# Performance work log

Measured on AMD Instinct MI355X. Metric: run time of the kernel, lower is better.

## Reference

```python
import jax, jax.numpy as jnp
import numpy as np

# Model dims (see init_kwargs)
B, S, D = 2, 2048, 2048          # batch, seq, hidden
H, HD = 16, 128                  # heads, head_dim (= ND + RD)
ND, RD = 64, 64                  # nope dim, rope dim per head
R = 512                          # kv lora rank
THETA = 10000.0


def _rotate_half(x):
    # interleaved rotation: pairs (x0,x1) -> (-x1, x0)
    x1 = x[..., ::2]
    x2 = x[..., 1::2]
    return jnp.stack((-x2, x1), axis=-1).reshape(x.shape)


def apply_rope(x, positions):
    # x: [..., seq, dim]
    dim = x.shape[-1]
    freqs = 1.0 / THETA ** (jnp.arange(0, dim, 2, dtype=x.dtype) / dim)  # [dim/2]
    angles = positions.astype(x.dtype)[:, None] * freqs                  # [seq, dim/2]
    cos = jnp.repeat(jnp.cos(angles), 2, axis=-1)[None, None]            # [1,1,seq,dim]
    sin = jnp.repeat(jnp.sin(angles), 2, axis=-1)[None, None]
    return x * cos + _rotate_half(x) * sin


def setup_inputs() -> dict:
    key = jax.random.key(0)
    ks = jax.random.split(key, 7)
    def lin(k, out_f, in_f):  # torch Linear convention: weight [out, in]
        return jax.random.normal(k, (out_f, in_f), dtype=jnp.float32) * (in_f ** -0.5)
    return {
        "x": jax.random.normal(ks[0], (B, S, D), dtype=jnp.float32),
        "wq": lin(ks[1], D, D),
        "w_kv_down": lin(ks[2], R, D),
        "w_k_up": lin(ks[3], H * ND, R),
        "w_k_rope": lin(ks[4], RD, D),
        "w_v_up": lin(ks[5], D, R),
        "wo": lin(ks[6], D, D),
    }


def reference(x, wq, w_kv_down, w_k_up, w_k_rope, w_v_up, wo):
    b, s, _ = x.shape
    pos = jnp.arange(s)
    scale = 1.0 / np.sqrt(HD).astype(np.float32)

    # queries: [b,H,s,HD] split into nope/rope parts, rope applied per head
    q = (x @ wq.T).reshape(b, s, H, HD).transpose(0, 2, 1, 3)
    q_nope = q[..., :ND]
    q_rope = apply_rope(q[..., ND:], pos)

    # compressed kv latent: [b,s,R]
    c_kv = x @ w_kv_down.T
    k_nope = (c_kv @ w_k_up.T).reshape(b, s, H, ND).transpose(0, 2, 1, 3)  # [b,H,s,ND]
    k_rope = apply_rope((x @ w_k_rope.T)[:, None], pos)[:, 0]             # [b,s,RD], shared across heads
    v = (c_kv @ w_v_up.T).reshape(b, s, H, HD).transpose(0, 2, 1, 3)      # [b,H,s,HD]

    # decomposed scores: nope part (per head) + rope part (shared k)
    scores = jnp.einsum('bhqd,bhkd->bhqk', q_nope, k_nope)
    scores = scores + jnp.einsum('bhqd,bkd->bhqk', q_rope, k_rope)
    scores = scores * scale

    causal = jnp.tril(jnp.ones((s, s), dtype=bool))
    scores = jnp.where(causal[None, None], scores, jnp.finfo(scores.dtype).min)
    attn = jax.nn.softmax(scores, axis=-1)

    out = jnp.einsum('bhqk,bhkd->bhqd', attn, v)
    out = out.transpose(0, 2, 1, 3).reshape(b, s, D)
    return out @ wo.T
```

## Files before the change

kernel.cpp:

```cpp
#include <hip/hip_runtime.h>
#include <stdint.h>


typedef unsigned short u16;
typedef __bf16 bf16x8 __attribute__((ext_vector_type(8)));
typedef float f32x4 __attribute__((ext_vector_type(4)));

#define QLD 2816

__device__ __forceinline__ float bf2f(u16 u) {
    union { unsigned int i; float f; } x; x.i = ((unsigned int)u) << 16; return x.f;
}
__device__ __forceinline__ u16 f2bf(float f) {
    union { float f; unsigned int i; } x; x.f = f;
    unsigned int r = x.i + 0x7fffu + ((x.i >> 16) & 1u);
    return (u16)(r >> 16);
}
__device__ __forceinline__ void store_c(u16* p, float v)  { *p = f2bf(v); }
__device__ __forceinline__ void store_c(float* p, float v){ *p = v; }

#define GLOBAL_AS __attribute__((address_space(1)))
#define LDS_AS    __attribute__((address_space(3)))
__device__ __forceinline__ void gl_lds16(const void* g, void* l) {
    __builtin_amdgcn_global_load_lds((GLOBAL_AS const void*)g, (LDS_AS void*)l, 16, 0, 0);
}

#if __has_builtin(__builtin_amdgcn_exp2f)
__device__ __forceinline__ float exp2fast(float x) { return __builtin_amdgcn_exp2f(x); }
#else
__device__ __forceinline__ float exp2fast(float x) { return __expf(x * 0.6931471805599453f); }
#endif

template<int CTRL>
__device__ __forceinline__ float fmax_dpp(float v) {
    int s = __builtin_bit_cast(int, v);
    int t = __builtin_amdgcn_update_dpp(s, s, CTRL, 0xF, 0xF, true);
    return fmaxf(v, __builtin_bit_cast(float, t));
}
__device__ __forceinline__ float rowmax16(float v) {
    v = fmax_dpp<0xB1>(v);
    v = fmax_dpp<0x4E>(v);
    v = fmax_dpp<0x124>(v);
    v = fmax_dpp<0x128>(v);
    return v;
}

__device__ __forceinline__ void cv8(const float* __restrict__ src,
                                    u16* __restrict__ dst, int i) {
    const float4* s = (const float4*)src;
    float4 v0 = s[2*i], v1 = s[2*i + 1];
    union { u16 u[8]; uint4 v; } o;
    o.u[0] = f2bf(v0.x); o.u[1] = f2bf(v0.y); o.u[2] = f2bf(v0.z); o.u[3] = f2bf(v0.w);
    o.u[4] = f2bf(v1.x); o.u[5] = f2bf(v1.y); o.u[6] = f2bf(v1.z); o.u[7] = f2bf(v1.w);
    *((uint4*)(dst + 8*i)) = o.v;
}

__global__ void convert_all(const float* __restrict__ s_x,
                            const float* __restrict__ s_wq,
                            const float* __restrict__ s_kvd,
                            const float* __restrict__ s_kup,
                            const float* __restrict__ s_vup,
                            const float* __restrict__ s_kr,
                            u16* __restrict__ xc, u16* __restrict__ wqcat,
                            u16* __restrict__ kupc, u16* __restrict__ vupc) {
    int i = blockIdx.x * 256 + threadIdx.x;
    if      (i < 1048576) cv8(s_x,   xc,                          i);
    else if (i < 1572864) cv8(s_wq,  wqcat,                       i - 1048576);
    else if (i < 1703936) cv8(s_kvd, wqcat + (size_t)2112*2048,   i - 1572864);
    else if (i < 1769472) cv8(s_kup, kupc,                        i - 1703936);
    else if (i < 1900544) cv8(s_vup, vupc,                        i - 1769472);
    else if (i < 1916928) cv8(s_kr,  wqcat + (size_t)2048*2048,   i - 1900544);
}

template<typename CT>
__global__ __launch_bounds__(512, 2)
void gemm256(const u16* __restrict__ A, const u16* __restrict__ W,
             CT* __restrict__ C, int K, int lda, int ldw, int ldc) {
    __shared__ u16 lds[4][16384];
    const int tid  = threadIdx.x;
    const int lane = tid & 63, l15 = lane & 15, quad = lane >> 4;
    const int wave = tid >> 6;
    const int wr = wave >> 2, wc = wave & 3;
    const int bm = blockIdx.y * 256;
    const int bn = blockIdx.x * 256;

    const int R = tid >> 2, slot = tid & 3;
    const int k16 = slot ^ ((R >> 1) & 3);
    const u16* asrc = A + (size_t)(bm + R) * lda + k16 * 8;
    const u16* bsrc = W + (size_t)(bn + R) * ldw + k16 * 8;
    const size_t astep = (size_t)128 * lda;
    const size_t bstep = (size_t)128 * ldw;

    #define STAGE256(st, bi) { \
        const u16* a0_ = asrc + (size_t)(st) * 32; \
        const u16* b0_ = bsrc + (size_t)(st) * 32; \
        gl_lds16(a0_,         &lds[bi][tid * 8]); \
        gl_lds16(a0_ + astep, &lds[bi][(tid + 512) * 8]); \
        gl_lds16(b0_,         &lds[bi][(tid + 1024) * 8]); \
        gl_lds16(b0_ + bstep, &lds[bi][(tid + 1536) * 8]); \
    }

    const f32x4 fzero = {0.f, 0.f, 0.f, 0.f};
    f32x4 acc[8][4];
    #pragma unroll
    for (int i = 0; i < 8; ++i)
        #pragma unroll
        for (int j = 0; j < 4; ++j) acc[i][j] = fzero;

    const int aswz = (quad ^ ((l15 >> 1) & 3)) * 8;

    const int nst = K >> 5;
    STAGE256(0, 0)
    STAGE256(1, 1)
    STAGE256(2, 2)
    asm volatile("s_waitcnt vmcnt(8)" ::: "memory");
    __builtin_amdgcn_s_barrier();

    for (int t = 0; t < nst; ++t) {
        const u16* buf = lds[t & 3];
        bf16x8 af[8], bfv[4];
        #pragma unroll
        for (int mf = 0; mf < 8; ++mf)
            af[mf] = *reinterpret_cast<const bf16x8*>(
                &buf[(wr*128 + mf*16 + l15)*32 + aswz]);
        #pragma unroll
        for (int nf = 0; nf < 4; ++nf)
            bfv[nf] = *reinterpret_cast<const bf16x8*>(
                &buf[8192 + (wc*64 + nf*16 + l15)*32 + aswz]);
        int st = t + 3; if (st > nst - 1) st = nst - 1;
        STAGE256(st, (t + 3) & 3)
        __builtin_amdgcn_s_setprio(1);
        #pragma unroll
        for (int mf = 0; mf < 8; ++mf)
            #pragma unroll
            for (int nf = 0; nf < 4; ++nf)
                acc[mf][nf] = __builtin_amdgcn_mfma_f32_16x16x32_bf16(
                    af[mf], bfv[nf], acc[mf][nf], 0, 0, 0);
        __builtin_amdgcn_s_setprio(0);
        asm volatile("s_waitcnt vmcnt(8) lgkmcnt(0)" ::: "memory");
        __builtin_amdgcn_sched_barrier(0);
        __builtin_amdgcn_s_barrier();
        __builtin_amdgcn_sched_barrier(0);
    }
    #undef STAGE256

    #pragma unroll
    for (int mf = 0; mf < 8; ++mf)
        #pragma unroll
        for (int nf = 0; nf < 4; ++nf)
            #pragma unroll
            for (int r = 0; r < 4; ++r) {
                int gm = bm + wr*128 + mf*16 + quad*4 + r;
                int gn = bn + wc*64 + nf*16 + l15;
                store_c(&C[(size_t)gm * ldc + gn], acc[mf][nf][r]);
            }
}

template<int EPI, typename CT>
__device__ __forceinline__ void gemm128_body(
        u16 (*lds)[12288],
        const u16* __restrict__ A, const u16* __restrict__ W,
        CT* __restrict__ C, int K, int lda, int ldw, int ldc,
        int bm, int bn) {
    const int tid  = threadIdx.x;
    const int lane = tid & 63, l15 = lane & 15, quad = lane >> 4;
    const int wave = tid >> 6;
    const int wr = wave >> 2, wc = wave & 3;

    const int R = tid >> 2, slot = tid & 3;
    const int k16 = slot ^ ((R >> 1) & 3);
    const u16* asrc = A + (size_t)(bm + R) * lda + k16 * 8;
    const u16* bsrc = W + (size_t)(bn + R) * ldw + k16 * 8;
    const size_t bstep = (size_t)128 * ldw;

    #define STAGE128(st, bi) { \
        const u16* a0_ = asrc + (size_t)(st) * 32; \
        const u16* b0_ = bsrc + (size_t)(st) * 32; \
        gl_lds16(a0_,         &lds[bi][tid * 8]); \
        gl_lds16(b0_,         &lds[bi][(tid + 512) * 8]); \
        gl_lds16(b0_ + bstep, &lds[bi][(tid + 1024) * 8]); \
    }

    const f32x4 fzero = {0.f, 0.f, 0.f, 0.f};
    f32x4 acc[4][4];
    #pragma unroll
    for (int i = 0; i < 4; ++i)
        #pragma unroll
        for (int j = 0; j < 4; ++j) acc[i][j] = fzero;

    const int aswz = (quad ^ ((l15 >> 1) & 3)) * 8;

    const int nst = K >> 5;
    STAGE128(0, 0)
    STAGE128(1, 1)
    asm volatile("s_waitcnt vmcnt(3)" ::: "memory");
    __builtin_amdgcn_s_barrier();

    int b0 = 0, bs = 2;
    for (int t = 0; t < nst; ++t) {
        const u16* buf = lds[b0];
        bf16x8 af[4], bfv[4];
        #pragma unroll
        for (int mf = 0; mf < 4; ++mf)
            af[mf] = *reinterpret_cast<const bf16x8*>(
                &buf[(wr*64 + mf*16 + l15)*32 + aswz]);
        #pragma unroll
        for (int nf = 0; nf < 4; ++nf)
            bfv[nf] = *reinterpret_cast<const bf16x8*>(
                &buf[4096 + (wc*64 + nf*16 + l15)*32 + aswz]);
        int st = t + 2; if (st > nst - 1) st = nst - 1;
        STAGE128(st, bs)
        __builtin_amdgcn_s_setprio(1);
        #pragma unroll
        for (int mf = 0; mf < 4; ++mf)
            #pragma unroll
            for (int nf = 0; nf < 4; ++nf)
                acc[mf][nf] = __builtin_amdgcn_mfma_f32_16x16x32_bf16(
                    af[mf], bfv[nf], acc[mf][nf], 0, 0, 0);
        __builtin_amdgcn_s_setprio(0);
        asm volatile("s_waitcnt vmcnt(3) lgkmcnt(0)" ::: "memory");
        __builtin_amdgcn_sched_barrier(0);
        __builtin_amdgcn_s_barrier();
        __builtin_amdgcn_sched_barrier(0);
        b0 = (b0 == 2) ? 0 : b0 + 1;
        bs = (bs == 2) ? 0 : bs + 1;
    }
    #undef STAGE128

    #pragma unroll
    for (int mf = 0; mf < 4; ++mf)
        #pragma unroll
        for (int nf = 0; nf < 4; ++nf)
            #pragma unroll
            for (int r = 0; r < 4; ++r) {
                int gm = bm + wr*64 + mf*16 + quad*4 + r;
                int gn = bn + wc*64 + nf*16 + l15;
                size_t ci;
                if (EPI == 1) ci = (size_t)gm*ldc + ((gn >> 6)*128 + (gn & 63));
                else          ci = (size_t)gm*ldc + gn;
                store_c(&C[ci], acc[mf][nf][r]);
            }
}

template<typename CT>
__global__ __launch_bounds__(512, 4)
void gemm128(const u16* __restrict__ A, const u16* __restrict__ W,
             CT* __restrict__ C, int K, int lda, int ldw, int ldc) {
    __shared__ u16 lds[3][12288];
    gemm128_body<0>(lds, A, W, C, K, lda, ldw, ldc,
                    (int)blockIdx.y * 128, (int)blockIdx.x * 256);
}

__global__ __launch_bounds__(512, 4)
void kv_up(const u16* __restrict__ ckv, const u16* __restrict__ kupc,
           u16* __restrict__ keff, const u16* __restrict__ vupc,
           u16* __restrict__ vT) {
    __shared__ u16 lds[3][12288];
    const int bx = blockIdx.x;
    if (bx < 128) {
        int bn = (bx & 3) * 256, bm = (bx >> 2) * 128;
        gemm128_body<1>(lds, ckv, kupc, keff, 512, QLD, 512, 2048, bm, bn);
    } else {
        int b2 = bx - 128;
        int bn = (b2 & 15) * 256, bm = (b2 >> 4) * 128;
        gemm128_body<0>(lds, vupc, ckv, vT, 512, 512, QLD, 4096, bm, bn);
    }
}

__global__ void rope_woc(u16* __restrict__ qcat, u16* __restrict__ keff,
                         const float* __restrict__ wo_src, u16* __restrict__ woc) {
    const int blk = blockIdx.x;
    if (blk >= 512) {
        int i = (blk - 512) * 256 + threadIdx.x;
        cv8(wo_src, woc, i);
        return;
    }
    int idx = blk * 256 + threadIdx.x;
    int i = idx & 31, r = idx >> 5;
    int pos = r & 2047;
    float freq = powf(10000.0f, -(float)i * (1.0f/32.0f));
    float ang  = (float)pos * freq;
    float s = sinf(ang), c = cosf(ang);

    u16* row = qcat + (size_t)r * QLD + 64 + 2*i;
    #pragma unroll
    for (int h = 0; h < 16; ++h) {
        unsigned int* p = (unsigned int*)(row + h*128);
        unsigned int v = *p;
        float x0 = bf2f((u16)(v & 0xffffu)), x1 = bf2f((u16)(v >> 16));
        unsigned int lo = f2bf(x0*c - x1*s);
        unsigned int hi = f2bf(x1*c + x0*s);
        *p = lo | (hi << 16);
    }

    const u16* p = qcat + (size_t)r * QLD + 2048 + 2*i;
    float x0 = bf2f(p[0]), x1 = bf2f(p[1]);
    union { u16 u[2]; unsigned int w; } o;
    o.u[0] = f2bf(x0*c - x1*s);
    o.u[1] = f2bf(x1*c + x0*s);
    unsigned int* base = (unsigned int*)(keff + (size_t)r*2048 + 64 + 2*i);
    #pragma unroll
    for (int h = 0; h < 16; ++h) base[h*64] = o.w;
}

__global__ __launch_bounds__(256, 3)
void attn_kernel(u16* __restrict__ qcat, const u16* __restrict__ KE,
                 const u16* __restrict__ VT) {
    constexpr int S = 2048;
    const int L = (int)blockIdx.y * 16 + (int)blockIdx.x;
    const int xcd = L & 7, j = L >> 3;
    const int bh   = xcd * 4 + (j & 3);
    const int pair = j >> 2;
    const int b = bh >> 4, h = bh & 15;

    __shared__ u16 Ks[64*128];
    __shared__ u16 Vs[128*64];
    __shared__ u16 Ps[64*68];

    const int tid  = threadIdx.x;
    const int lane = tid & 63, l15 = lane & 15, quad = lane >> 4;
    const int wave = tid >> 6;

    const u16* ksrc[4];
    const u16* vsrc[4];
    #pragma unroll
    for (int i = 0; i < 4; ++i) {
        int g = tid + i*256;
        {
            int r = g >> 4, slot = g & 15, cg = slot ^ (r & 15);
            ksrc[i] = KE + (size_t)(b*S + r)*2048 + h*128 + cg*8;
        }
        {
            int d = g >> 3, slot = g & 7, cg = slot ^ (d & 7);
            vsrc[i] = VT + (size_t)(h*128 + d)*4096 + (size_t)(b*S) + cg*8;
        }
    }

    bf16x8 kreg[4], vreg[4];
    #pragma unroll
    for (int i = 0; i < 4; ++i) {
        kreg[i] = *reinterpret_cast<const bf16x8*>(ksrc[i]);
        vreg[i] = *reinterpret_cast<const bf16x8*>(vsrc[i]);
    }

    union { u16 u[8]; bf16x8 v; } onesu;
    #pragma unroll
    for (int i = 0; i < 8; ++i) onesu.u[i] = 0x3f80;
    const bf16x8 ones = onesu.v;

    const f32x4 fzero = {0.f, 0.f, 0.f, 0.f};
    const float NEG = -1e30f;
    const float KLOG = 0.12751739f;
    const float THR = 8.0f;

    __bf16* PsB = reinterpret_cast<__bf16*>(Ps);

    for (int half = 0; half < 2; ++half) {
        const int qt = half ? pair : 31 - pair;
        const int nkt = qt + 1;

        u16* qbase = qcat + (size_t)(b*S + qt*64) * QLD + h*128;
        bf16x8 aq[4];
        #pragma unroll
        for (int ks = 0; ks < 4; ++ks)
            aq[ks] = *reinterpret_cast<const bf16x8*>(
                qbase + (size_t)(wave*16 + l15)*QLD + ks*32 + quad*8);

        float m2[4]  = {NEG, NEG, NEG, NEG};
        float l_i[4] = {0.f, 0.f, 0.f, 0.f};
        f32x4 oacc[8];
        #pragma unroll
        for (int i = 0; i < 8; ++i) oacc[i] = fzero;

        const int qrow0 = qt*64 + wave*16 + quad*4;

        for (int kt = 0; kt < nkt; ++kt) {
            const bool is_last = (kt == nkt - 1);
            #pragma unroll
            for (int i = 0; i < 4; ++i) {
                *reinterpret_cast<bf16x8*>(&Ks[(tid + i*256) * 8]) = kreg[i];
                *reinterpret_cast<bf16x8*>(&Vs[(tid + i*256) * 8]) = vreg[i];
            }
            {
                int ktn = (kt + 1 < nkt) ? kt + 1 : 0;
                #pragma unroll
                for (int i = 0; i < 4; ++i) {
                    kreg[i] = *reinterpret_cast<const bf16x8*>(ksrc[i] + (size_t)ktn*(64*2048));
                    vreg[i] = *reinterpret_cast<const bf16x8*>(vsrc[i] + (size_t)ktn*64);
                }
            }
            __syncthreads();

            f32x4 sfr[4];
            __builtin_amdgcn_s_setprio(1);
            #pragma unroll
            for (int nt = 0; nt < 4; ++nt) {
                f32x4 s = fzero;
                int n = nt*16 + l15;
                #pragma unroll
                for (int ks = 0; ks < 4; ++ks) {
                    int c = ks*4 + quad;
                    bf16x8 bk = *reinterpret_cast<const bf16x8*>(&Ks[n*128 + ((c ^ l15) * 8)]);
                    s = __builtin_amdgcn_mfma_f32_16x16x32_bf16(aq[ks], bk, s, 0, 0, 0);
                }
                sfr[nt] = s;
            }
            __builtin_amdgcn_s_setprio(0);
            if (is_last) {
                #pragma unroll
                for (int nt = 0; nt < 4; ++nt) {
                    int kg = kt*64 + nt*16 + l15;
                    #pragma unroll
                    for (int r = 0; r < 4; ++r)
                        if (kg > qrow0 + r) sfr[nt][r] = NEG;
                }
            }
            float rm[4];
            #pragma unroll
            for (int r = 0; r < 4; ++r) {
                rm[r] = fmaxf(fmaxf(sfr[0][r], sfr[1][r]), fmaxf(sfr[2][r], sfr[3][r]));
                rm[r] = rowmax16(rm[r]);
            }
            float c2[4];
            int need = 0;
            #pragma unroll
            for (int r = 0; r < 4; ++r) {
                c2[r] = rm[r] * KLOG;
                need |= (c2[r] > m2[r] + THR) ? 1 : 0;
            }
            if (__any(need)) {
                float alpha[4];
                #pragma unroll
                for (int r = 0; r < 4; ++r) {
                    float mn = fmaxf(m2[r], c2[r]);
                    alpha[r] = exp2fast(m2[r] - mn);
                    m2[r] = mn;
                    l_i[r] *= alpha[r];
                }
                #pragma unroll
                for (int i = 0; i < 8; ++i)
                    #pragma unroll
                    for (int r = 0; r < 4; ++r)
                        oacc[i][r] *= alpha[r];
            }
            float pf[4][4];
            #pragma unroll
            for (int nt = 0; nt < 4; ++nt)
                #pragma unroll
                for (int r = 0; r < 4; ++r)
                    pf[nt][r] = exp2fast(__builtin_fmaf(sfr[nt][r], KLOG, -m2[r]));

            #pragma unroll
            for (int nt = 0; nt < 4; ++nt) {
                int base = (wave*16 + quad*4)*68 + nt*16 + l15;
                #pragma unroll
                for (int r = 0; r < 4; ++r)
                    PsB[base + r*68] = (__bf16)pf[nt][r];
            }

            f32x4 lfr = fzero;
            __builtin_amdgcn_s_setprio(1);
            #pragma unroll
            for (int ks = 0; ks < 2; ++ks) {
                bf16x8 pa = *reinterpret_cast<const bf16x8*>(
                    &Ps[(wave*16 + l15)*68 + ks*32 + quad*8]);
                lfr = __builtin_amdgcn_mfma_f32_16x16x32_bf16(pa, ones, lfr, 0, 0, 0);
                #pragma unroll
                for (int ntv = 0; ntv < 8; ++ntv) {
                    int c = ks*4 + quad;
                    bf16x8 bv = *reinterpret_cast<const bf16x8*>(
                        &Vs[(ntv*16 + l15)*64 + ((c ^ (l15 & 7)) * 8)]);
                    oacc[ntv] = __builtin_amdgcn_mfma_f32_16x16x32_bf16(pa, bv, oacc[ntv], 0, 0, 0);
                }
            }
            __builtin_amdgcn_s_setprio(0);
            #pragma unroll
            for (int r = 0; r < 4; ++r) l_i[r] += lfr[r];
            __syncthreads();
        }

        #pragma unroll
        for (int r = 0; r < 4; ++r) {
            float inv = 1.0f / l_i[r];
            int qrow = wave*16 + quad*4 + r;
            #pragma unroll
            for (int ntv = 0; ntv < 8; ++ntv) {
                int d = ntv*16 + l15;
                qbase[(size_t)qrow*QLD + d] = f2bf(oacc[ntv][r] * inv);
            }
        }
    }
}

extern "C" void kernel_launch(void* const* d_in, const int* in_sizes, int n_in,
                              void* d_out, int out_size, void* d_ws, size_t ws_size,
                              hipStream_t stream) {
    (void)in_sizes; (void)n_in; (void)out_size; (void)ws_size;
    float* out = (float*)d_out;
    char* ws = (char*)d_ws;

    u16* xc     = (u16*)(ws);
    u16* qcat   = (u16*)(ws + 16777216);
    u16* keff   = (u16*)(ws + 39845888);
    u16* wqcat  = (u16*)(ws + 56623104);
    u16* kupc   = (u16*)(ws + 68157440);
    u16* vupc   = (u16*)(ws + 69206016);
    u16* vT     = xc;
    u16* woc    = wqcat;

    convert_all<<<7488, 256, 0, stream>>>(
        (const float*)d_in[0], (const float*)d_in[1], (const float*)d_in[2],
        (const float*)d_in[3], (const float*)d_in[5], (const float*)d_in[4],
        xc, wqcat, kupc, vupc);

    gemm256<u16><<<dim3(11, 16), 512, 0, stream>>>(
        xc, wqcat, qcat, 2048, 2048, 2048, QLD);

    rope_woc<<<2560, 256, 0, stream>>>(qcat, keff, (const float*)d_in[6], woc);

    kv_up<<<384, 512, 0, stream>>>(qcat + 2112, kupc, keff, vupc, vT);

    attn_kernel<<<dim3(16, 32), 256, 0, stream>>>(qcat, keff, vT);

    gemm128<float><<<dim3(8, 32), 512, 0, stream>>>(
        qcat, woc, out, 2048, QLD, 2048, 2048);
}
```

Before: 310.5 us.

## Load V fragments directly from global into registers, dropping LDS staging of V

```diff
diff --git a/kernel.cpp b/kernel.cpp
--- a/kernel.cpp
+++ b/kernel.cpp
@@ -303,7 +303,7 @@
     for (int h = 0; h < 16; ++h) base[h*64] = o.w;
 }
 
-__global__ __launch_bounds__(256, 3)
+__global__ __launch_bounds__(256, 2)
 void attn_kernel(u16* __restrict__ qcat, const u16* __restrict__ KE,
                  const u16* __restrict__ VT) {
     constexpr int S = 2048;
@@ -314,7 +314,6 @@
     const int b = bh >> 4, h = bh & 15;
 
     __shared__ u16 Ks[64*128];
-    __shared__ u16 Vs[128*64];
     __shared__ u16 Ps[64*68];
 
     const int tid  = threadIdx.x;
@@ -322,26 +321,19 @@
     const int wave = tid >> 6;
 
     const u16* ksrc[4];
-    const u16* vsrc[4];
     #pragma unroll
     for (int i = 0; i < 4; ++i) {
         int g = tid + i*256;
-        {
-            int r = g >> 4, slot = g & 15, cg = slot ^ (r & 15);
-            ksrc[i] = KE + (size_t)(b*S + r)*2048 + h*128 + cg*8;
-        }
-        {
-            int d = g >> 3, slot = g & 7, cg = slot ^ (d & 7);
-            vsrc[i] = VT + (size_t)(h*128 + d)*4096 + (size_t)(b*S) + cg*8;
-        }
-    }
-
-    bf16x8 kreg[4], vreg[4];
-    #pragma unroll
-    for (int i = 0; i < 4; ++i) {
+        int r = g >> 4, slot = g & 15, cg = slot ^ (r & 15);
+        ksrc[i] = KE + (size_t)(b*S + r)*2048 + h*128 + cg*8;
+    }
+
+    const u16* vb = VT + (size_t)(h*128 + l15)*4096 + (size_t)(b*S) + quad*8;
+
+    bf16x8 kreg[4];
+    #pragma unroll
+    for (int i = 0; i < 4; ++i)
         kreg[i] = *reinterpret_cast<const bf16x8*>(ksrc[i]);
-        vreg[i] = *reinterpret_cast<const bf16x8*>(vsrc[i]);
-    }
 
     union { u16 u[8]; bf16x8 v; } onesu;
     #pragma unroll
@@ -377,17 +369,22 @@
         for (int kt = 0; kt < nkt; ++kt) {
             const bool is_last = (kt == nkt - 1);
             #pragma unroll
-            for (int i = 0; i < 4; ++i) {
+            for (int i = 0; i < 4; ++i)
                 *reinterpret_cast<bf16x8*>(&Ks[(tid + i*256) * 8]) = kreg[i];
-                *reinterpret_cast<bf16x8*>(&Vs[(tid + i*256) * 8]) = vreg[i];
-            }
+
+            bf16x8 vfr[2][8];
+            #pragma unroll
+            for (int ks = 0; ks < 2; ++ks)
+                #pragma unroll
+                for (int ntv = 0; ntv < 8; ++ntv)
+                    vfr[ks][ntv] = *reinterpret_cast<const bf16x8*>(
+                        vb + (size_t)ntv*65536 + kt*64 + ks*32);
+
             {
                 int ktn = (kt + 1 < nkt) ? kt + 1 : 0;
                 #pragma unroll
-                for (int i = 0; i < 4; ++i) {
+                for (int i = 0; i < 4; ++i)
                     kreg[i] = *reinterpret_cast<const bf16x8*>(ksrc[i] + (size_t)ktn*(64*2048));
-                    vreg[i] = *reinterpret_cast<const bf16x8*>(vsrc[i] + (size_t)ktn*64);
-                }
             }
             __syncthreads();
 
@@ -466,12 +463,9 @@
                     &Ps[(wave*16 + l15)*68 + ks*32 + quad*8]);
                 lfr = __builtin_amdgcn_mfma_f32_16x16x32_bf16(pa, ones, lfr, 0, 0, 0);
                 #pragma unroll
-                for (int ntv = 0; ntv < 8; ++ntv) {
-                    int c = ks*4 + quad;
-                    bf16x8 bv = *reinterpret_cast<const bf16x8*>(
-                        &Vs[(ntv*16 + l15)*64 + ((c ^ (l15 & 7)) * 8)]);
-                    oacc[ntv] = __builtin_amdgcn_mfma_f32_16x16x32_bf16(pa, bv, oacc[ntv], 0, 0, 0);
-                }
+                for (int ntv = 0; ntv < 8; ++ntv)
+                    oacc[ntv] = __builtin_amdgcn_mfma_f32_16x16x32_bf16(
+                        pa, vfr[ks][ntv], oacc[ntv], 0, 0, 0);
             }
             __builtin_amdgcn_s_setprio(0);
             #pragma unroll
```

Result: slower. 394.6 us (+27.1%).
